# Performance work log

Hardware: AMD Instinct MI355X
Metric: run time of the kernel (lower is better)

The kernel has to match this reference:

```python
import jax, jax.numpy as jnp
import numpy as np

D = 2  # spatial dimension


def conv_contract(x, filt, k_in, k_out):
    """Equivariant convolve-then-contract for one (in,out) type pair.
    x: (B, Cin, H, W) + (D,)*k_in
    filt: (O, Cin, 3, 3) + (D,)*k_in + (D,)*k_out
    The first k_in tensor indices of the filter contract with the image's
    tensor indices (absorbed into the conv's input-feature dimension).
    Torus (periodic) padding, stride 1, as per padding='TORUS'.
    """
    B, Cin, H, W = x.shape[0], x.shape[1], x.shape[2], x.shape[3]
    O = filt.shape[0]
    din, dout = D ** k_in, D ** k_out
    # fold tensor-in components into input channels: (B, Cin*din, H, W)
    xr = jnp.moveaxis(x.reshape(B, Cin, H, W, din), -1, 2).reshape(B, Cin * din, H, W)
    # filter -> (O*dout, Cin*din, 3, 3) with matching (Cin, din) ordering
    fr = filt.reshape(O, Cin, 3, 3, din, dout)
    fr = jnp.transpose(fr, (0, 5, 1, 4, 2, 3)).reshape(O * dout, Cin * din, 3, 3)
    # periodic padding then VALID conv == TORUS padding
    xp = jnp.pad(xr, ((0, 0), (0, 0), (1, 1), (1, 1)), mode='wrap')
    out = jax.lax.conv_general_dilated(xp, fr, (1, 1), 'VALID',
                                       dimension_numbers=('NCHW', 'OIHW', 'NCHW'))
    out = jnp.moveaxis(out.reshape(B, O, dout, H, W), 2, -1)  # (B,O,H,W,dout)
    return out.reshape((B, O, H, W) + (D,) * k_out)


def setup_inputs() -> dict:
    key = jax.random.key(0)
    ks = jax.random.split(key, 11)
    B, Cin, Cout, H, W = 8, 96, 96, 128, 128
    N0, N1, N2 = 3, 4, 5  # num invariant filters for tensor order 0,1,2
    b0 = 1.0 / np.sqrt(Cin * 9)
    b1 = 1.0 / np.sqrt(Cin * 9 * D)
    inp = {
        'x_scalar': jax.random.normal(ks[0], (B, Cin, H, W), dtype=jnp.float32),
        'x_vector': jax.random.normal(ks[1], (B, Cin, H, W, D), dtype=jnp.float32),
        'f_k0': jax.random.normal(ks[2], (N0, 3, 3), dtype=jnp.float32),
        'f_k1': jax.random.normal(ks[3], (N1, 3, 3, D), dtype=jnp.float32),
        'f_k2': jax.random.normal(ks[4], (N2, 3, 3, D, D), dtype=jnp.float32),
        'w_ss': jax.random.uniform(ks[5], (Cout, Cin, N0), minval=-b0, maxval=b0),
        'w_sv': jax.random.uniform(ks[6], (Cout, Cin, N1), minval=-b0, maxval=b0),
        'w_vs': jax.random.uniform(ks[7], (Cout, Cin, N1), minval=-b1, maxval=b1),
        'w_vv': jax.random.uniform(ks[8], (Cout, Cin, N2), minval=-b1, maxval=b1),
        'b_s': jax.random.uniform(ks[9], (Cout, 1, 1), minval=-b0, maxval=b0),
        'b_v': jax.random.uniform(ks[10], (Cout, 1, 1, 1), minval=-b1, maxval=b1),
    }
    return inp


def reference(x_scalar, x_vector, f_k0, f_k1, f_k2, w_ss, w_sv, w_vs, w_vv, b_s, b_v):
    # build per-pair filters: weights (O,I,N) x invariant filters (N, 3,3, D^k...)
    f_k0 = jax.lax.stop_gradient(f_k0)
    f_k1 = jax.lax.stop_gradient(f_k1)
    f_k2 = jax.lax.stop_gradient(f_k2)
    F_ss = jnp.einsum('oin,nhw->oihw', w_ss, f_k0)        # scalar->scalar
    F_sv = jnp.einsum('oin,nhwa->oihwa', w_sv, f_k1)      # scalar->vector
    F_vs = jnp.einsum('oin,nhwa->oihwa', w_vs, f_k1)      # vector->scalar
    F_vv = jnp.einsum('oin,nhwab->oihwab', w_vv, f_k2)    # vector->vector
    # convolve each input type against each output type, contract in-tensor
    # indices, and sum contributions per output type
    out_s = conv_contract(x_scalar, F_ss, 0, 0) + conv_contract(x_vector, F_vs, 1, 0)
    out_v = conv_contract(x_scalar, F_sv, 0, 1) + conv_contract(x_vector, F_vv, 1, 1)
    # use_bias='auto': regular bias for scalars, mean-scaled bias for non-scalars
    out_s = out_s + b_s[None]
    out_v = out_v + b_v[None] * jnp.mean(out_v, axis=(2, 3), keepdims=True)
    return out_s, out_v
```

## Files before the change

kernel.cpp:

```cpp
#include <hip/hip_runtime.h>

#define HWSZ 16384
#define CIN 96
#define ICTOT 288
#define OUT_S_ELEMS (8*96*16384)
#define TILE_USH (ICTOT*32)
#define NTILES 81

typedef __attribute__((ext_vector_type(8))) short bf16x8;
typedef __attribute__((ext_vector_type(4))) float f32x4;

#define VMCNT(n) asm volatile("s_waitcnt vmcnt(" #n ")" ::: "memory")

__device__ __forceinline__ unsigned short f2bf(float f){
  unsigned int u = __float_as_uint(f);
  u += 0x7FFFu + ((u >> 16) & 1u);
  return (unsigned short)(u >> 16);
}

__device__ __forceinline__ void gload16(const unsigned short* g, const unsigned short* l){
  __builtin_amdgcn_global_load_lds(
      (const __attribute__((address_space(1))) unsigned int*)g,
      (__attribute__((address_space(3))) unsigned int*)l, 16, 0, 0);
}

__global__ void pack_w_kernel(const float* __restrict__ w_ss, const float* __restrict__ w_sv,
                              const float* __restrict__ w_vs, const float* __restrict__ w_vv,
                              const float* __restrict__ f_k0, const float* __restrict__ f_k1,
                              const float* __restrict__ f_k2, unsigned short* __restrict__ WbT){
  int idx = blockIdx.x*256 + threadIdx.x;
  if (idx >= NTILES*ICTOT*32) return;
  int j = idx / (ICTOT*32); int rem = idx - j*(ICTOT*32);
  int oc = rem >> 5, cc = rem & 31;
  int tap = j % 9, cch = j / 9;
  int ic = cch*32 + cc;
  float acc = 0.f;
  if (oc < 96){
    int o = oc;
    if (ic < CIN){
      int i = ic;
      for (int n=0;n<3;++n) acc += w_ss[(o*CIN+i)*3+n]*f_k0[n*9+tap];
    } else {
      int v = ic-CIN; int i=v>>1, a=v&1;
      for (int n=0;n<4;++n) acc += w_vs[(o*CIN+i)*4+n]*f_k1[(n*9+tap)*2+a];
    }
  } else {
    int ov = oc-96; int o=ov>>1, c=ov&1;
    if (ic < CIN){
      int i = ic;
      for (int n=0;n<4;++n) acc += w_sv[(o*CIN+i)*4+n]*f_k1[(n*9+tap)*2+c];
    } else {
      int v = ic-CIN; int i=v>>1, a=v&1;
      for (int n=0;n<5;++n) acc += w_vv[(o*CIN+i)*5+n]*f_k2[((n*9+tap)*2+a)*2+c];
    }
  }
  int cc_sw = ((((cc>>3) ^ ((oc>>1)&3)) << 3) | (cc & 7));
  WbT[(size_t)j*TILE_USH + oc*32 + cc_sw] = f2bf(acc);
}

__global__ void pack_x_kernel(const float* __restrict__ xs, const float* __restrict__ xv,
                              unsigned short* __restrict__ Xp, float* __restrict__ Part){
  __shared__ float2 tile[32][65];
  __shared__ float red[2][8][32];
  int bid0 = blockIdx.x;
  int t = threadIdx.x;
  if (bid0 < 6144){
    int bid = bid0;
    int ct = bid % 3; int pt = (bid/3) & 255; int b = bid / 768;
    int p0 = pt*64, c0 = ct*32;
    float* tf = (float*)tile;
    int cl = t >> 6, pl = t & 63;
    for (int kk=0; kk<8; ++kk){
      int c = kk*4 + cl;
      tf[c*130 + pl] = xs[(size_t)(b*CIN + c0 + c)*HWSZ + p0 + pl];
    }
    __syncthreads();
    int c = t & 31, pw = t >> 5;
    float psum = 0.f;
    for (int j=0;j<8;++j){
      int p = pw*8 + j;
      float v = tf[c*130 + p];
      psum += v;
      Xp[(size_t)(b*HWSZ + p0 + p)*ICTOT + c0 + c] = f2bf(v);
    }
    red[0][pw][c] = psum;
    __syncthreads();
    if (t < 32){
      float s = 0.f;
      #pragma unroll
      for (int k=0;k<8;++k) s += red[0][k][t];
      Part[((size_t)b*ICTOT + c0 + t)*256 + pt] = s;
    }
  } else {
    int bid = bid0 - 6144;
    int ct = bid % 3; int pt = (bid/3) & 255; int b = bid / 768;
    int p0 = pt*64, c0 = ct*32;
    int cl = t >> 6, pl = t & 63;
    const float2* src = (const float2*)xv;
    for (int kk=0; kk<8; ++kk){
      int c = kk*4 + cl;
      tile[c][pl] = src[(size_t)(b*CIN + c0 + c)*HWSZ + p0 + pl];
    }
    __syncthreads();
    int c = t & 31, pw = t >> 5;
    float sx = 0.f, sy = 0.f;
    for (int j=0;j<8;++j){
      int p = pw*8 + j;
      float2 v = tile[c][p];
      sx += v.x; sy += v.y;
      unsigned int u = (unsigned int)f2bf(v.x) | ((unsigned int)f2bf(v.y) << 16);
      *(unsigned int*)&Xp[(size_t)(b*HWSZ + p0 + p)*ICTOT + CIN + 2*(c0+c)] = u;
    }
    red[0][pw][c] = sx; red[1][pw][c] = sy;
    __syncthreads();
    if (t < 32){
      float s0 = 0.f, s1 = 0.f;
      #pragma unroll
      for (int k=0;k<8;++k){ s0 += red[0][k][t]; s1 += red[1][k][t]; }
      Part[((size_t)b*ICTOT + CIN + 2*(c0+t)    )*256 + pt] = s0;
      Part[((size_t)b*ICTOT + CIN + 2*(c0+t) + 1)*256 + pt] = s1;
    }
  }
}

__global__ void reduce_part_kernel(const float* __restrict__ Part, float* __restrict__ Ssum){
  int b = blockIdx.x;
  int t = threadIdx.x;
  if (t >= ICTOT) return;
  const float* p = Part + ((size_t)b*ICTOT + t)*256;
  float s = 0.f;
  #pragma unroll 8
  for (int i=0;i<256;++i) s += p[i];
  Ssum[b*ICTOT + t] = s;
}

__global__ void mbias_kernel(const float* __restrict__ w_sv, const float* __restrict__ w_vv,
                             const float* __restrict__ f_k1, const float* __restrict__ f_k2,
                             const float* __restrict__ b_v, const float* __restrict__ Ssum,
                             float* __restrict__ MB){
  int row = blockIdx.x;
  int o = row >> 1, c = row & 1;
  int lane = threadIdx.x;
  float f1s[4], f2s[5][2];
  for (int n=0;n<4;++n){
    float s=0.f;
    for (int tap=0;tap<9;++tap) s += f_k1[(n*9+tap)*2+c];
    f1s[n]=s;
  }
  for (int n=0;n<5;++n)
    for (int a=0;a<2;++a){
      float s=0.f;
      for (int tap=0;tap<9;++tap) s += f_k2[((n*9+tap)*2+a)*2+c];
      f2s[n][a]=s;
    }
  float wv[5];
  for (int k=0;k<5;++k){
    int ic = lane + 64*k;
    float v = 0.f;
    if (ic < CIN){
      for (int n=0;n<4;++n) v += w_sv[(o*CIN+ic)*4+n]*f1s[n];
    } else if (ic < ICTOT){
      int u = ic-CIN; int i=u>>1, a=u&1;
      for (int n=0;n<5;++n) v += w_vv[(o*CIN+i)*5+n]*f2s[n][a];
    }
    wv[k] = v;
  }
  for (int b=0;b<8;++b){
    float acc = 0.f;
    for (int k=0;k<5;++k){
      int ic = lane + 64*k;
      if (ic < ICTOT) acc += wv[k]*Ssum[b*ICTOT+ic];
    }
    for (int m=1;m<64;m<<=1) acc += __shfl_xor(acc, m);
    if (lane == 0) MB[b*192+row] = b_v[o]*acc*(1.f/16384.f);
  }
}

__global__ __launch_bounds__(512,2) void conv_mfma_kernel(
    const unsigned short* __restrict__ Xp, const unsigned short* __restrict__ WbT,
    const float* __restrict__ b_s, const float* __restrict__ MB,
    float* __restrict__ out){
  __shared__ unsigned short Ash[3][1536*8];
  __shared__ unsigned short Bsh[2][2048*8];

  int bid = blockIdx.x;
  int b = bid & 7, rp = bid >> 3;
  int tid = threadIdx.x;
  int lane = tid & 63, w = tid >> 6;
  int wr = w >> 2, wc = w & 3;
  int cl = lane & 15, g = lane >> 4;

  f32x4 acc[9][4];
  #pragma unroll
  for (int m=0;m<9;++m)
    #pragma unroll
    for (int n=0;n<4;++n) acc[m][n] = (f32x4){0.f,0.f,0.f,0.f};

  const size_t xb = (size_t)b * HWSZ * ICTOT;
  const unsigned short* srcB[4];
  #pragma unroll
  for (int i=0;i<4;++i){
    int f = i*512 + tid;
    int j = f >> 9, px = (f >> 2) & 127, cp = f & 3;
    int cps = cp ^ ((px >> 1) & 3);
    int hs = (2*rp - 1 + j + 128) & 127;
    srcB[i] = Xp + xb + ((size_t)(hs*128 + px))*ICTOT + cps*8;
  }
  const unsigned short* srcA = WbT + tid*8;
  const int wlds = w*64*8;
  const int Abase = (wr*144 + cl)*32 + ((g ^ ((cl>>1)&3))*8);
  const int pxb = (wc & 1)*64 + cl;
  const int jr0 = (wc >> 1);

  int boff[12];
  #pragma unroll
  for (int kx=0;kx<3;++kx)
    #pragma unroll
    for (int n=0;n<4;++n){
      int px = (pxb + n*16 + kx + 127) & 127;
      boff[kx*4+n] = px*32 + ((g ^ ((px >> 1) & 3))*8);
    }

  #pragma unroll
  for (int i=0;i<4;++i) gload16(srcB[i], &Bsh[0][i*4096 + wlds]);
  #pragma unroll
  for (int i=0;i<3;++i) gload16(srcA + 0*TILE_USH + i*4096, &Ash[0][i*4096 + wlds]);
  #pragma unroll
  for (int i=0;i<3;++i) gload16(srcA + 1*TILE_USH + i*4096, &Ash[1][i*4096 + wlds]);
  VMCNT(0);
  __builtin_amdgcn_s_barrier();

  bf16x8 afc[9], bfc[4];
  #pragma unroll
  for (int n=0;n<4;++n) bfc[n] = *(const bf16x8*)&Bsh[0][jr0*4096 + boff[0*4+n]];
  #pragma unroll
  for (int m=0;m<9;++m) afc[m] = *(const bf16x8*)&Ash[0][Abase + m*512];

  const unsigned short* cA = srcA;
  for (int c = 0; c < 9; ++c){
    const unsigned short* Bcur = Bsh[c & 1];
    unsigned short* Bnxt = (unsigned short*)Bsh[(c & 1) ^ 1];
    #pragma unroll
    for (int t = 0; t < 9; ++t){
      if (c < 8 || t <= 6){
        #pragma unroll
        for (int i=0;i<3;++i)
          gload16(cA + (t+2)*TILE_USH + i*4096, &Ash[(t+2)%3][i*4096 + wlds]);
      }
      if (t == 0 && c < 8){
        #pragma unroll
        for (int i=0;i<4;++i)
          gload16(srcB[i] + (c+1)*32, &Bnxt[i*4096 + wlds]);
      }
      if (c < 8){ if (t <= 1) { VMCNT(7); } else { VMCNT(3); } }
      else      { if (t <= 6) { VMCNT(3); } else if (t == 7) { VMCNT(0); } }
      const unsigned short* Anxt = Ash[(t+1)%3];
      __builtin_amdgcn_s_setprio(1);
      #pragma unroll
      for (int m=0;m<9;++m){
        #pragma unroll
        for (int n=0;n<4;++n)
          acc[m][n] = __builtin_amdgcn_mfma_f32_16x16x32_bf16(afc[m], bfc[n], acc[m][n], 0,0,0);
        if (c < 8 || t < 8){
          afc[m] = *(const bf16x8*)&Anxt[Abase + m*512];
          __builtin_amdgcn_sched_group_barrier(0x008, 4, 0);
          __builtin_amdgcn_sched_group_barrier(0x100, 1, 0);
        } else {
          __builtin_amdgcn_sched_group_barrier(0x008, 4, 0);
        }
      }
      __builtin_amdgcn_s_setprio(0);
      if (c < 8 || t < 8){
        const int tau = (t+1)%9;
        const int ky = tau/3, kx = tau%3;
        const unsigned short* Bsrc = (t < 8 ? Bcur : (const unsigned short*)Bnxt) + (jr0 + ky)*4096;
        #pragma unroll
        for (int n=0;n<4;++n) bfc[n] = *(const bf16x8*)&Bsrc[boff[kx*4+n]];
      }
      __builtin_amdgcn_sched_barrier(0);
      __builtin_amdgcn_s_barrier();
    }
    cA += 9*TILE_USH;
  }

  const int orow = 2*rp + (wc >> 1);
  const int colb = (wc & 1)*64;
  #pragma unroll
  for (int m=0;m<9;++m){
    int ocb = wr*144 + m*16 + 4*g;
    if (wr == 0 && m < 6){
      #pragma unroll
      for (int r=0;r<4;++r){
        int oc = ocb + r;
        float bias = b_s[oc];
        #pragma unroll
        for (int n=0;n<4;++n){
          int p = orow*128 + colb + n*16 + cl;
          out[(size_t)(b*96+oc)*HWSZ + p] = acc[m][n][r] + bias;
        }
      }
    } else {
      float2* outv = (float2*)(out + OUT_S_ELEMS);
      int row0 = ocb - 96;
      int o0 = row0 >> 1;
      float mb0 = MB[b*192+row0  ], mb1 = MB[b*192+row0+1];
      float mb2 = MB[b*192+row0+2], mb3 = MB[b*192+row0+3];
      #pragma unroll
      for (int n=0;n<4;++n){
        int p = orow*128 + colb + n*16 + cl;
        outv[(size_t)(b*96+o0  )*HWSZ + p] = (float2){acc[m][n][0]+mb0, acc[m][n][1]+mb1};
        outv[(size_t)(b*96+o0+1)*HWSZ + p] = (float2){acc[m][n][2]+mb2, acc[m][n][3]+mb3};
      }
    }
  }
}

extern "C" void kernel_launch(void* const* d_in, const int* in_sizes, int n_in,
                              void* d_out, int out_size, void* d_ws, size_t ws_size,
                              hipStream_t stream){
  const float* xs   = (const float*)d_in[0];
  const float* xv   = (const float*)d_in[1];
  const float* f_k0 = (const float*)d_in[2];
  const float* f_k1 = (const float*)d_in[3];
  const float* f_k2 = (const float*)d_in[4];
  const float* w_ss = (const float*)d_in[5];
  const float* w_sv = (const float*)d_in[6];
  const float* w_vs = (const float*)d_in[7];
  const float* w_vv = (const float*)d_in[8];
  const float* b_s  = (const float*)d_in[9];
  const float* b_v  = (const float*)d_in[10];
  float* out = (float*)d_out;

  char* ws = (char*)d_ws;
  unsigned short* WbT = (unsigned short*)ws;
  const size_t XP_OFF = (size_t)NTILES*TILE_USH*2 + 6144;
  unsigned short* Xp = (unsigned short*)(ws + XP_OFF);
  const size_t PART_OFF = XP_OFF + (size_t)8*HWSZ*ICTOT*2;
  float* Part = (float*)(ws + PART_OFF);
  float* Ssum = (float*)(ws + PART_OFF + 2359296);
  float* MB   = (float*)(ws + PART_OFF + 2359296 + 9216);

  pack_w_kernel<<<(NTILES*ICTOT*32 + 255)/256, 256, 0, stream>>>(
      w_ss, w_sv, w_vs, w_vv, f_k0, f_k1, f_k2, WbT);
  pack_x_kernel<<<12288, 256, 0, stream>>>(xs, xv, Xp, Part);
  reduce_part_kernel<<<8, 320, 0, stream>>>(Part, Ssum);
  mbias_kernel<<<192, 64, 0, stream>>>(w_sv, w_vv, f_k1, f_k2, b_v, Ssum, MB);
  conv_mfma_kernel<<<512, 512, 0, stream>>>(Xp, WbT, b_s, MB, out);
}
```

Baseline: 244.9 us.

## Deepen weight-tile ring to four stages and barrier every other step

```diff
diff --git a/kernel.cpp b/kernel.cpp
--- a/kernel.cpp
+++ b/kernel.cpp
@@ -180,8 +180,8 @@
     const unsigned short* __restrict__ Xp, const unsigned short* __restrict__ WbT,
     const float* __restrict__ b_s, const float* __restrict__ MB,
     float* __restrict__ out){
-  __shared__ unsigned short Ash[3][1536*8];
-  __shared__ unsigned short Bsh[2][2048*8];
+  __shared__ unsigned short Ash[4][9216];
+  __shared__ unsigned short Bsh[2][16384];
 
   int bid = blockIdx.x;
   int b = bid & 7, rp = bid >> 3;
@@ -189,6 +189,7 @@
   int lane = tid & 63, w = tid >> 6;
   int wr = w >> 2, wc = w & 3;
   int cl = lane & 15, g = lane >> 4;
+  const bool wlt2 = (tid < 128);
 
   f32x4 acc[9][4];
   #pragma unroll
@@ -206,8 +207,7 @@
     int hs = (2*rp - 1 + j + 128) & 127;
     srcB[i] = Xp + xb + ((size_t)(hs*128 + px))*ICTOT + cps*8;
   }
-  const unsigned short* srcA = WbT + tid*8;
-  const int wlds = w*64*8;
+  const int wls = w*512;
   const int Abase = (wr*144 + cl)*32 + ((g ^ ((cl>>1)&3))*8);
   const int pxb = (wc & 1)*64 + cl;
   const int jr0 = (wc >> 1);
@@ -222,65 +222,73 @@
     }
 
   #pragma unroll
-  for (int i=0;i<4;++i) gload16(srcB[i], &Bsh[0][i*4096 + wlds]);
-  #pragma unroll
-  for (int i=0;i<3;++i) gload16(srcA + 0*TILE_USH + i*4096, &Ash[0][i*4096 + wlds]);
-  #pragma unroll
-  for (int i=0;i<3;++i) gload16(srcA + 1*TILE_USH + i*4096, &Ash[1][i*4096 + wlds]);
+  for (int i=0;i<4;++i) gload16(srcB[i], &Bsh[0][i*4096 + wls]);
+  #pragma unroll
+  for (int j=0;j<3;++j){
+    const unsigned short* s = WbT + (size_t)j*TILE_USH;
+    unsigned short* d = &Ash[j][0];
+    gload16(s + tid*8,        d + wls);
+    gload16(s + 4096 + tid*8, d + 4096 + wls);
+    if (tid < 128) gload16(s + 8192 + tid*8, d + 8192 + wls);
+  }
   VMCNT(0);
   __builtin_amdgcn_s_barrier();
 
   bf16x8 afc[9], bfc[4];
   #pragma unroll
-  for (int n=0;n<4;++n) bfc[n] = *(const bf16x8*)&Bsh[0][jr0*4096 + boff[0*4+n]];
+  for (int n=0;n<4;++n) bfc[n] = *(const bf16x8*)&Bsh[0][jr0*4096 + boff[n]];
   #pragma unroll
   for (int m=0;m<9;++m) afc[m] = *(const bf16x8*)&Ash[0][Abase + m*512];
 
-  const unsigned short* cA = srcA;
   for (int c = 0; c < 9; ++c){
     const unsigned short* Bcur = Bsh[c & 1];
     unsigned short* Bnxt = (unsigned short*)Bsh[(c & 1) ^ 1];
+    const unsigned short* cA = WbT + (size_t)(9*c)*TILE_USH;
     #pragma unroll
     for (int t = 0; t < 9; ++t){
-      if (c < 8 || t <= 6){
-        #pragma unroll
-        for (int i=0;i<3;++i)
-          gload16(cA + (t+2)*TILE_USH + i*4096, &Ash[(t+2)%3][i*4096 + wlds]);
+      if (c < 8 || t <= 5){
+        const unsigned short* s = cA + (size_t)(t+3)*TILE_USH;
+        unsigned short* d = &Ash[(c + t + 3) & 3][0];
+        gload16(s + tid*8,        d + wls);
+        gload16(s + 4096 + tid*8, d + 4096 + wls);
+        if (tid < 128) gload16(s + 8192 + tid*8, d + 8192 + wls);
       }
       if (t == 0 && c < 8){
         #pragma unroll
         for (int i=0;i<4;++i)
-          gload16(srcB[i] + (c+1)*32, &Bnxt[i*4096 + wlds]);
-      }
-      if (c < 8){ if (t <= 1) { VMCNT(7); } else { VMCNT(3); } }
-      else      { if (t <= 6) { VMCNT(3); } else if (t == 7) { VMCNT(0); } }
-      const unsigned short* Anxt = Ash[(t+1)%3];
+          gload16(srcB[i] + (c+1)*32, &Bnxt[i*4096 + wls]);
+      }
       __builtin_amdgcn_s_setprio(1);
       #pragma unroll
       for (int m=0;m<9;++m){
         #pragma unroll
         for (int n=0;n<4;++n)
           acc[m][n] = __builtin_amdgcn_mfma_f32_16x16x32_bf16(afc[m], bfc[n], acc[m][n], 0,0,0);
-        if (c < 8 || t < 8){
-          afc[m] = *(const bf16x8*)&Anxt[Abase + m*512];
-          __builtin_amdgcn_sched_group_barrier(0x008, 4, 0);
-          __builtin_amdgcn_sched_group_barrier(0x100, 1, 0);
-        } else {
-          __builtin_amdgcn_sched_group_barrier(0x008, 4, 0);
-        }
       }
       __builtin_amdgcn_s_setprio(0);
+      if (c < 8){
+        if (t <= 1){ if (wlt2) { VMCNT(10); } else { VMCNT(8); } }
+        else       { if (wlt2) { VMCNT(6);  } else { VMCNT(4); } }
+      } else {
+        if (t <= 5)      { if (wlt2) { VMCNT(6); } else { VMCNT(4); } }
+        else if (t == 6) { if (wlt2) { VMCNT(3); } else { VMCNT(2); } }
+        else if (t == 7) { VMCNT(0); }
+      }
       if (c < 8 || t < 8){
         const int tau = (t+1)%9;
         const int ky = tau/3, kx = tau%3;
         const unsigned short* Bsrc = (t < 8 ? Bcur : (const unsigned short*)Bnxt) + (jr0 + ky)*4096;
         #pragma unroll
         for (int n=0;n<4;++n) bfc[n] = *(const bf16x8*)&Bsrc[boff[kx*4+n]];
-      }
-      __builtin_amdgcn_sched_barrier(0);
-      __builtin_amdgcn_s_barrier();
-    }
-    cA += 9*TILE_USH;
+        const unsigned short* At = &Ash[(c + t + 1) & 3][0];
+        #pragma unroll
+        for (int m=0;m<9;++m) afc[m] = *(const bf16x8*)&At[Abase + m*512];
+      }
+      if (((c + t) & 1) == 1){
+        __builtin_amdgcn_sched_barrier(0);
+        __builtin_amdgcn_s_barrier();
+      }
+    }
   }
 
   const int orow = 2*rp + (wc >> 1);
```

Measured after the change: 270.8 us. 1.11x slower.
